# Optimization experiments

Measured on AMD Instinct MI355X. Metric: run time of the kernel, lower is better.

The kernel has to match this reference:

```python
import jax, jax.numpy as jnp
import numpy as np

HID = 128      # hidden_dim (= head_dim since num_heads = 1)
NR = 64        # num_radial
CUT = 10.0     # cutoff
K = 32         # k_neighbors
E = 8192       # number of edges
N = 2048       # number of nodes
DIN = 2 * HID + NR + 1  # attention MLP input dim
LN_EPS = 1e-5


def setup_inputs() -> dict:
    key = jax.random.key(0)
    ks = jax.random.split(key, 16)
    def lin(k, i, o):
        # xavier-ish scaling
        return (jax.random.normal(k, (i, o), jnp.float32) / np.sqrt(i)).astype(jnp.float32)
    return {
        "edge_features": jax.random.normal(ks[0], (E, HID), jnp.float32),
        "edge_coords": jax.random.normal(ks[1], (E, 3), jnp.float32),
        "node_coords": jax.random.normal(ks[2], (N, 3), jnp.float32) * 3.0,
        "Wq": lin(ks[4], HID, HID), "Wk": lin(ks[5], HID, HID), "Wv": lin(ks[6], HID, HID),
        "W1": lin(ks[7], DIN, HID), "b1": jnp.zeros((HID,), jnp.float32),
        "W2": lin(ks[8], HID, HID), "b2": jnp.zeros((HID,), jnp.float32),
        "W3": lin(ks[9], HID, 1), "b3": jnp.zeros((1,), jnp.float32),
        "Wg1": lin(ks[10], HID, HID), "bg1": jnp.zeros((HID,), jnp.float32),
        "Wg2": lin(ks[11], HID, 1), "bg2": jnp.zeros((1,), jnp.float32),
        "Wo": lin(ks[12], HID, HID), "bo": jnp.zeros((HID,), jnp.float32),
        "gamma": jnp.ones((HID,), jnp.float32), "beta": jnp.zeros((HID,), jnp.float32),
        "centers": jnp.linspace(0.0, CUT, NR, dtype=jnp.float32),
        "widths": jnp.full((NR,), 0.5, jnp.float32),
        "edge_index": jax.random.randint(ks[3], (2, E), 0, N, jnp.int32),
    }


def _forward(ef, ec, nc, Wq, Wk, Wv, W1, b1, W2, b2, W3, b3,
             Wg1, bg1, Wg2, bg2, Wo, bo, gamma, beta, centers, widths, edge_index):
    silu = jax.nn.silu
    # edge center coordinates: [E,3]
    cen = (nc[edge_index[0]] + nc[edge_index[1]]) * 0.5
    # pairwise squared distances via gram trick (monotone in distance -> same topk)
    n2 = jnp.sum(cen * cen, axis=-1)
    d2 = n2[:, None] + n2[None, :] - 2.0 * (cen @ cen.T)          # [E,E]
    _, idx = jax.lax.top_k(-d2, K)                                # [E,K] nearest edge centers
    # gathered geometry
    coord_diff = cen[:, None, :] - cen[idx]                       # [E,K,3]
    dist = jnp.sqrt(jnp.sum(coord_diff * coord_diff, axis=-1))    # [E,K]
    in_cut = dist <= CUT                                          # [E,K]
    # RBF (cutoff mask applied as in RadialBasisFunction)
    rbf = jnp.exp(-widths * (dist[..., None] - centers) ** 2) * in_cut[..., None].astype(jnp.float32)  # [E,K,NR]
    # projections (num_heads = 1 -> head_dim = HID)
    q = ef @ Wq                                                   # [E,HID]
    k = ef @ Wk
    v = ef @ Wv
    kj = k[idx]                                                   # [E,K,HID]
    dot = jnp.einsum('ed,ekd->ek', q, kj)                         # [E,K]
    # attention MLP on [q_i, k_j, rbf, dot]
    qb = jnp.broadcast_to(q[:, None, :], (E, K, HID))
    mlp_in = jnp.concatenate([qb, kj, rbf, dot[..., None]], axis=-1)  # [E,K,DIN]
    h = silu(mlp_in @ W1 + b1)
    h = silu(h @ W2 + b2)
    raw = (h @ W3 + b3)[..., 0]                                   # [E,K]
    # scores: MLP output inside cutoff, else left at 0 (as in the torch loop)
    scores = jnp.where(in_cut, raw, 0.0)
    # softmax over the FULL row of length E: the (E-K) non-neighbor entries are 0
    m = jnp.maximum(jnp.max(scores, axis=1), 0.0)                 # [E]
    ex = jnp.exp(scores - m[:, None])                             # [E,K]
    Z = jnp.sum(ex, axis=1) + (E - K) * jnp.exp(-m)               # [E]
    w = ex / Z[:, None]                                           # [E,K] weights at neighbors only
    # feature update: only neighbor entries are accumulated
    weighted_v = jnp.einsum('ek,ekd->ed', w, v[idx])              # [E,HID]
    updated = ef + weighted_v
    # coordinate gates from v
    gates = jax.nn.sigmoid(silu(v @ Wg1 + bg1) @ Wg2 + bg2)       # [E,1]
    gj = gates[idx][..., 0]                                       # [E,K]
    coord_update = jnp.einsum('ek,ekc->ec', w * gj, coord_diff)   # [E,3]
    updated_coords = ec + coord_update
    # output projection + residual + LayerNorm
    x = ef + (updated @ Wo + bo)
    mu = jnp.mean(x, axis=-1, keepdims=True)
    var = jnp.mean((x - mu) ** 2, axis=-1, keepdims=True)
    feat_out = (x - mu) * jax.lax.rsqrt(var + LN_EPS) * gamma + beta
    return feat_out, updated_coords


def reference(edge_features, edge_coords, node_coords, Wq, Wk, Wv, W1, b1, W2, b2, W3, b3,
              Wg1, bg1, Wg2, bg2, Wo, bo, gamma, beta, centers, widths, edge_index):
    return _forward(edge_features, edge_coords, node_coords, Wq, Wk, Wv, W1, b1, W2, b2,
                    W3, b3, Wg1, bg1, Wg2, bg2, Wo, bo, gamma, beta, centers, widths, edge_index)
```

## Files before the change

kernel.cpp:

```cpp
#include <hip/hip_runtime.h>
#include <math.h>

#define E_N   8192
#define HID   128
#define NRAD  64
#define KNB   32
#define CUTF  10.0f
#define LNEPS 1e-5f

typedef unsigned short u16;
typedef unsigned int   u32;
typedef unsigned long long u64;
typedef __bf16 bf16x8 __attribute__((ext_vector_type(8)));
typedef u16    u16x8  __attribute__((ext_vector_type(8)));
typedef float  f32x4  __attribute__((ext_vector_type(4)));

__device__ __forceinline__ u16 f2bf(float f) {
  __bf16 h = (__bf16)f;
  return __builtin_bit_cast(u16, h);
}
__device__ __forceinline__ float bf2f(u16 v) {
  return __uint_as_float(((u32)v) << 16);
}

__device__ __forceinline__ u64 shflx64(u64 v, int m) {
  int lo = __shfl_xor((int)(v & 0xffffffffull), m, 64);
  int hi = __shfl_xor((int)(v >> 32), m, 64);
  return ((u64)(unsigned)hi << 32) | (unsigned)lo;
}

__device__ __forceinline__ u32 d2key(const float4 me, const float4 c) {
  float dot = fmaf(me.x, c.x, fmaf(me.y, c.y, me.z * c.z));
  float d2  = fmaf(-2.0f, dot, me.w + c.w);
  u32 u = __float_as_uint(d2);
  return u ^ (((u32)((int)u >> 31)) | 0x80000000u);
}

__global__ __launch_bounds__(256) void k_pre(
    const float* __restrict__ W1, const float* __restrict__ W2,
    const float* __restrict__ Wq, const float* __restrict__ Wk,
    const float* __restrict__ Wv, const float* __restrict__ Wg1,
    const float* __restrict__ nc, const int* __restrict__ ei,
    u16* __restrict__ Wt1r, u16* __restrict__ Wt2,
    u16* __restrict__ Wqt, u16* __restrict__ Wkt, u16* __restrict__ Wvt,
    u16* __restrict__ Wqct, u16* __restrict__ Wkct, u16* __restrict__ Wvgt,
    float4* __restrict__ cen4) {
  const int b = blockIdx.x, t = threadIdx.x;
  if (b < 128) {
    if (t < 64)       Wt1r[b*64 + t]      = f2bf(W1[(256+t)*HID + b]);
    else if (t < 192) Wt2[b*HID + (t-64)] = f2bf(W2[(t-64)*HID + b]);
  } else if (b < 256) {
    const int r = b - 128, o = t & 127;
    float a = 0.f;
    if (t < 128) {
      #pragma unroll 8
      for (int m = 0; m < 128; ++m) a = fmaf(Wq[r*128+m], W1[m*128+o], a);
      Wqct[o*128 + r] = f2bf(a);
    } else {
      #pragma unroll 8
      for (int m = 0; m < 128; ++m) a = fmaf(Wk[r*128+m], W1[(128+m)*128+o], a);
      Wkct[o*128 + r] = f2bf(a);
    }
  } else if (b < 384) {
    const int r = b - 256;
    if (t < 128) {
      float a = 0.f;
      #pragma unroll 8
      for (int m = 0; m < 128; ++m) a = fmaf(Wv[r*128+m], Wg1[m*128+t], a);
      Wvgt[t*128 + r] = f2bf(a);
    }
  } else if (b < 512) {
    const int c = b - 384;
    if (t < 128) Wqt[c*128 + t]       = f2bf(Wq[t*128 + c]);
    else         Wkt[c*128 + (t-128)] = f2bf(Wk[(t-128)*128 + c]);
  } else if (b < 640) {
    const int c = b - 512;
    if (t < 128) Wvt[c*128 + t] = f2bf(Wv[t*128 + c]);
  } else {
    const int e = (b - 640)*256 + t;
    if (e < E_N) {
      int a = ei[e], bb = ei[E_N + e];
      float x = (nc[a*3+0] + nc[bb*3+0]) * 0.5f;
      float y = (nc[a*3+1] + nc[bb*3+1]) * 0.5f;
      float z = (nc[a*3+2] + nc[bb*3+2]) * 0.5f;
      cen4[e] = make_float4(x, y, z, x*x + y*y + z*z);
    }
  }
}

__global__ __launch_bounds__(256) void k_topk(const float4* __restrict__ cen4,
                                              int* __restrict__ idxo) {
  const int row0 = blockIdx.x * 8;
  const int t = threadIdx.x;
  const int lane = t & 63, w = t >> 6;
  __shared__ __align__(16) u32 smin[8][256];
  __shared__ __align__(16) u64 comp[2048];
  __shared__ u32 sU[8];
  __shared__ u32 scnt, scnt_r[8];
  __shared__ u64 wred[4];
  __shared__ u64 winner;

  if (t == 0) scnt = 0;
  if (t < 8) scnt_r[t] = 0;

  float4 me[8];
  #pragma unroll
  for (int r = 0; r < 8; ++r) me[r] = cen4[row0 + r];

  u32 mn[8];
  #pragma unroll
  for (int r = 0; r < 8; ++r) mn[r] = 0xFFFFFFFFu;
  for (int s = 0; s < 32; ++s) {
    float4 c = cen4[t + (s << 8)];
    #pragma unroll
    for (int r = 0; r < 8; ++r) {
      u32 k = d2key(me[r], c);
      mn[r] = k < mn[r] ? k : mn[r];
    }
  }
  #pragma unroll
  for (int r = 0; r < 8; ++r) smin[r][t] = mn[r];
  __syncthreads();

  #pragma unroll
  for (int rr = 0; rr < 2; ++rr) {
    const int r = w*2 + rr;
    uint4 vv = *(const uint4*)&smin[r][lane*4];
    u32 P = 0;
    u32 rem = 31;
    #pragma unroll 1
    for (int b = 31; b >= 12; --b) {
      u32 bit = 1u << b;
      bool pm0 = ((u64)(vv.x ^ P) >> (b+1)) == 0ull;
      bool pm1 = ((u64)(vv.y ^ P) >> (b+1)) == 0ull;
      bool pm2 = ((u64)(vv.z ^ P) >> (b+1)) == 0ull;
      bool pm3 = ((u64)(vv.w ^ P) >> (b+1)) == 0ull;
      u32 c0 = (u32)__popcll(__ballot(pm0 && !(vv.x & bit)))
             + (u32)__popcll(__ballot(pm1 && !(vv.y & bit)))
             + (u32)__popcll(__ballot(pm2 && !(vv.z & bit)))
             + (u32)__popcll(__ballot(pm3 && !(vv.w & bit)));
      if (rem >= c0) { P |= bit; rem -= c0; }
    }
    if (lane == 0) sU[r] = P | 0xFFFu;
  }
  __syncthreads();

  u32 Ur[8];
  #pragma unroll
  for (int r = 0; r < 8; ++r) Ur[r] = sU[r];
  for (int s = 0; s < 32; ++s) {
    float4 c = cen4[t + (s << 8)];
    #pragma unroll
    for (int r = 0; r < 8; ++r) {
      u32 k = d2key(me[r], c);
      if (k <= Ur[r]) {
        u32 pos = atomicAdd(&scnt, 1u);
        atomicAdd(&scnt_r[r], 1u);
        if (pos < 2048u)
          comp[pos] = ((u64)r << 45) | (((u64)k) << 13) | (u32)(t + (s << 8));
      }
    }
  }
  __syncthreads();
  const int cnt = (int)scnt;

  if (cnt <= 2048) {
    u32 off[8];
    off[0] = 0;
    #pragma unroll
    for (int r = 1; r < 8; ++r) off[r] = off[r-1] + scnt_r[r-1];
    for (int i = t; i < cnt; i += 256) {
      u64 mev = comp[i];
      int rk = 0;
      int j2 = 0;
      for (; j2 + 2 <= cnt; j2 += 2) {
        ulonglong2 pr = *(const ulonglong2*)&comp[j2];
        rk += (pr.x < mev) ? 1 : 0;
        rk += (pr.y < mev) ? 1 : 0;
      }
      if (j2 < cnt) rk += (comp[j2] < mev) ? 1 : 0;
      int r = (int)(mev >> 45);
      int rank = rk - (int)off[r];
      if (rank < KNB) idxo[(row0 + r)*KNB + rank] = (int)(mev & 0x1FFFull);
    }
  } else {
    for (int r = 0; r < 8; ++r) {
      float4 mer = cen4[row0 + r];
      u32 taken = 0;
      for (int kk2 = 0; kk2 < KNB; ++kk2) {
        u64 lk = 0xFFFFFFFFFFFFFFFFull;
        for (int s = 0; s < 32; ++s) {
          if (taken & (1u << s)) continue;
          float4 c = cen4[t + (s << 8)];
          u64 kx = (((u64)d2key(mer, c)) << 13) | (u32)(t + (s << 8));
          lk = kx < lk ? kx : lk;
        }
        #pragma unroll
        for (int m = 1; m < 64; m <<= 1) {
          u64 o = shflx64(lk, m);
          lk = o < lk ? o : lk;
        }
        if (lane == 0) wred[w] = lk;
        __syncthreads();
        if (t == 0) {
          u64 w0 = wred[0] < wred[1] ? wred[0] : wred[1];
          u64 w1 = wred[2] < wred[3] ? wred[2] : wred[3];
          winner = w0 < w1 ? w0 : w1;
          idxo[(row0 + r)*KNB + kk2] = (int)(winner & 0x1FFFull);
        }
        __syncthreads();
        u64 jw = winner & 0x1FFFull;
        if (((u32)jw & 255u) == (u32)t) taken |= 1u << ((u32)jw >> 8);
        __syncthreads();
      }
    }
  }
}

__global__ __launch_bounds__(256) void k_qkv(const float* __restrict__ ef,
    const u16* __restrict__ Wqt, const u16* __restrict__ Wkt, const u16* __restrict__ Wvt,
    const u16* __restrict__ Wqct, const u16* __restrict__ Wkct, const u16* __restrict__ Wvgt,
    const float* __restrict__ b1, const float* __restrict__ bg1,
    const float* __restrict__ Wg2, const float* __restrict__ bg2,
    float* __restrict__ qf, float* __restrict__ qW1,
    u16* __restrict__ kjp, u16* __restrict__ vfb, float* __restrict__ gates) {
  __shared__ u16 sE[32*128];
  __shared__ float spart[4][32];
  const int t = threadIdx.x;
  const int w = t >> 6, l = t & 63;
  const int l15 = l & 15, l4 = l >> 4;
  const int e0 = blockIdx.x * 32;
  const int colw = w * 32;

  {
    const int srow = t >> 3, sb = t & 7;
    const float4* src = (const float4*)(ef + (size_t)(e0 + srow)*HID + sb*16);
    #pragma unroll
    for (int g = 0; g < 2; ++g) {
      float4 v0 = src[g*2], v1 = src[g*2+1];
      u16x8 vv;
      vv[0]=f2bf(v0.x); vv[1]=f2bf(v0.y); vv[2]=f2bf(v0.z); vv[3]=f2bf(v0.w);
      vv[4]=f2bf(v1.x); vv[5]=f2bf(v1.y); vv[6]=f2bf(v1.z); vv[7]=f2bf(v1.w);
      int widx = (srow*128 + sb*16 + g*8) ^ ((srow & 7) << 3);
      *(u16x8*)(&sE[widx]) = vv;
    }
  }
  __syncthreads();

  bf16x8 afq[2][4];
  #pragma unroll
  for (int rt = 0; rt < 2; ++rt) {
    int row = rt*16 + l15;
    #pragma unroll
    for (int ks = 0; ks < 4; ++ks) {
      int aidx = (row*128 + ks*32 + l4*8) ^ ((row & 7) << 3);
      afq[rt][ks] = *(const bf16x8*)(&sE[aidx]);
    }
  }

  f32x4 a2[2][2];
  auto gemm_panel = [&](const u16* __restrict__ P) {
    #pragma unroll
    for (int rt = 0; rt < 2; ++rt)
      #pragma unroll
      for (int ct = 0; ct < 2; ++ct) a2[rt][ct] = (f32x4){0.f,0.f,0.f,0.f};
    #pragma unroll
    for (int ks = 0; ks < 4; ++ks) {
      bf16x8 bfr[2];
      #pragma unroll
      for (int ct = 0; ct < 2; ++ct)
        bfr[ct] = *(const bf16x8*)(&P[(colw + ct*16 + l15)*128 + ks*32 + l4*8]);
      #pragma unroll
      for (int rt = 0; rt < 2; ++rt)
        #pragma unroll
        for (int ct = 0; ct < 2; ++ct)
          a2[rt][ct] = __builtin_amdgcn_mfma_f32_16x16x32_bf16(afq[rt][ks], bfr[ct], a2[rt][ct], 0, 0, 0);
    }
  };

  gemm_panel(Wqt);
  #pragma unroll
  for (int rt = 0; rt < 2; ++rt)
    #pragma unroll
    for (int r = 0; r < 4; ++r) {
      size_t e = e0 + rt*16 + l4*4 + r;
      #pragma unroll
      for (int ct = 0; ct < 2; ++ct)
        qf[e*HID + colw + ct*16 + l15] = a2[rt][ct][r];
    }
  gemm_panel(Wkt);
  #pragma unroll
  for (int rt = 0; rt < 2; ++rt)
    #pragma unroll
    for (int r = 0; r < 4; ++r) {
      size_t e = e0 + rt*16 + l4*4 + r;
      #pragma unroll
      for (int ct = 0; ct < 2; ++ct)
        kjp[e*256 + 128 + colw + ct*16 + l15] = f2bf(a2[rt][ct][r]);
    }
  gemm_panel(Wvt);
  #pragma unroll
  for (int rt = 0; rt < 2; ++rt)
    #pragma unroll
    for (int r = 0; r < 4; ++r) {
      size_t e = e0 + rt*16 + l4*4 + r;
      #pragma unroll
      for (int ct = 0; ct < 2; ++ct)
        vfb[e*HID + colw + ct*16 + l15] = f2bf(a2[rt][ct][r]);
    }
  gemm_panel(Wqct);
  {
    float b1r[2];
    #pragma unroll
    for (int ct = 0; ct < 2; ++ct) b1r[ct] = b1[colw + ct*16 + l15];
    #pragma unroll
    for (int rt = 0; rt < 2; ++rt)
      #pragma unroll
      for (int r = 0; r < 4; ++r) {
        size_t e = e0 + rt*16 + l4*4 + r;
        #pragma unroll
        for (int ct = 0; ct < 2; ++ct)
          qW1[e*HID + colw + ct*16 + l15] = a2[rt][ct][r] + b1r[ct];
      }
  }
  gemm_panel(Wkct);
  #pragma unroll
  for (int rt = 0; rt < 2; ++rt)
    #pragma unroll
    for (int r = 0; r < 4; ++r) {
      size_t e = e0 + rt*16 + l4*4 + r;
      #pragma unroll
      for (int ct = 0; ct < 2; ++ct)
        kjp[e*256 + colw + ct*16 + l15] = f2bf(a2[rt][ct][r]);
    }
  gemm_panel(Wvgt);
  {
    float bgr[2], w3r[2];
    #pragma unroll
    for (int ct = 0; ct < 2; ++ct) {
      int col = colw + ct*16 + l15;
      bgr[ct] = bg1[col]; w3r[ct] = Wg2[col];
    }
    #pragma unroll
    for (int rt = 0; rt < 2; ++rt)
      #pragma unroll
      for (int r = 0; r < 4; ++r) {
        float part = 0.f;
        #pragma unroll
        for (int ct = 0; ct < 2; ++ct) {
          float x = a2[rt][ct][r] + bgr[ct];
          float g = x / (1.0f + __expf(-x));
          part = fmaf(g, w3r[ct], part);
        }
        part += __shfl_xor(part, 1, 64);
        part += __shfl_xor(part, 2, 64);
        part += __shfl_xor(part, 4, 64);
        part += __shfl_xor(part, 8, 64);
        if (l15 == 0) spart[w][rt*16 + l4*4 + r] = part;
      }
  }
  __syncthreads();
  if (t < 32)
    gates[e0 + t] = 1.0f / (1.0f + __expf(-(spart[0][t] + spart[1][t] + spart[2][t] + spart[3][t] + bg2[0])));
}

__global__ __launch_bounds__(512) void k_mega(
    const int* __restrict__ idx,
    const float* __restrict__ qf,
    const float4* __restrict__ cen4,
    const float* __restrict__ qW1, const u16* __restrict__ kjp,
    const u16* __restrict__ vfb, const float* __restrict__ gates,
    const u16* __restrict__ Wt1r, const u16* __restrict__ Wt2,
    const float* __restrict__ W1,
    const float* __restrict__ b2, const float* __restrict__ W3,
    const float* __restrict__ b3,
    const float* __restrict__ centers, const float* __restrict__ widths,
    const float* __restrict__ ef, const float* __restrict__ ec,
    const float* __restrict__ Wo, const float* __restrict__ bo,
    const float* __restrict__ gamma, const float* __restrict__ beta,
    float* __restrict__ outf, float* __restrict__ outc) {
  __shared__ u16 sH[128*128];
  __shared__ u16 sA[128*64];
  float* spart = (float*)sA;
  float* sUpd  = (float*)sA + 512;
  float* swk   = (float*)sA + 1024;
  float* sred  = (float*)sA + 1152;
  __shared__ float sQW[4][128];
  __shared__ float sDot[128];
  __shared__ float sDist[128];
  __shared__ int   sIdx[128];

  const int t  = threadIdx.x;
  const int w  = t >> 6, l = t & 63;
  const int l15 = l & 15, l4 = l >> 4;
  const int c4 = w & 3, rh = w >> 2;
  const int rowbase = blockIdx.x * 128;
  const int eBase = rowbase >> 5;

  const int srow = t >> 2, sb = t & 3;
  const int sp = rowbase + srow;
  const int se = sp >> 5;
  const int sj = idx[sp];
  {
    const u16x8* kw = (const u16x8*)(kjp + (size_t)sj*256 + sb*32);
    #pragma unroll
    for (int g = 0; g < 4; ++g) {
      int widx = (srow*128 + sb*32 + g*8) ^ ((srow & 7) << 3);
      *(u16x8*)(&sH[widx]) = kw[g];
    }
  }
  const u16x8* kb = (const u16x8*)(kjp + (size_t)sj*256 + 128 + sb*32);
  const float4* q4 = (const float4*)(qf + (size_t)se*HID) + sb*8;
  float dt = 0.f;
  #pragma unroll
  for (int i = 0; i < 4; ++i) {
    u16x8 kv8 = kb[i];
    float4 qa = q4[i*2], qb = q4[i*2+1];
    dt += bf2f(kv8[0])*qa.x + bf2f(kv8[1])*qa.y + bf2f(kv8[2])*qa.z + bf2f(kv8[3])*qa.w
        + bf2f(kv8[4])*qb.x + bf2f(kv8[5])*qb.y + bf2f(kv8[6])*qb.z + bf2f(kv8[7])*qb.w;
  }
  dt += __shfl_xor(dt, 1, 64);
  dt += __shfl_xor(dt, 2, 64);
  float4 ce = cen4[se], cj = cen4[sj];
  float ddx = ce.x - cj.x, ddy = ce.y - cj.y, ddz = ce.z - cj.z;
  const float sdist = sqrtf(ddx*ddx + ddy*ddy + ddz*ddz);
  const float sincut = (sdist <= CUTF) ? 1.0f : 0.0f;
  if (sb == 0) { sDot[srow] = dt; sDist[srow] = sdist; }
  {
    u16 tmp[16];
    #pragma unroll
    for (int i4 = 0; i4 < 4; ++i4) {
      float4 cc = *(const float4*)(centers + sb*16 + i4*4);
      float4 ww = *(const float4*)(widths  + sb*16 + i4*4);
      float c4v[4] = {cc.x,cc.y,cc.z,cc.w}, w4[4] = {ww.x,ww.y,ww.z,ww.w};
      #pragma unroll
      for (int jj = 0; jj < 4; ++jj) {
        float df = sdist - c4v[jj];
        tmp[i4*4+jj] = f2bf(__expf(-w4[jj]*df*df) * sincut);
      }
    }
    #pragma unroll
    for (int g = 0; g < 2; ++g) {
      u16x8 vv;
      #pragma unroll
      for (int jj = 0; jj < 8; ++jj) vv[jj] = tmp[g*8+jj];
      int widx = (srow*64 + sb*16 + g*8) ^ ((srow & 7) << 3);
      *(u16x8*)(&sA[widx]) = vv;
    }
  }
  sQW[t >> 7][t & 127] = qW1[(size_t)(eBase + (t >> 7))*HID + (t & 127)];
  if (t < 128) sIdx[t] = idx[rowbase + t];

  u32 vp[16];
  {
    const int eh2 = t >> 7, colp = t & 127;
    const int ib = rowbase + eh2*32;
    #pragma unroll
    for (int kk = 0; kk < 16; ++kk) {
      int j0 = idx[ib + 2*kk], j1 = idx[ib + 2*kk + 1];
      u32 a = vfb[(size_t)j0*HID + colp];
      u32 b = vfb[(size_t)j1*HID + colp];
      vp[kk] = a | (b << 16);
    }
  }
  __syncthreads();

  f32x4 acc[4][2];
  #pragma unroll
  for (int rt = 0; rt < 4; ++rt)
    #pragma unroll
    for (int ct = 0; ct < 2; ++ct) acc[rt][ct] = (f32x4){0.f,0.f,0.f,0.f};

  #pragma unroll
  for (int ks = 0; ks < 2; ++ks) {
    bf16x8 af[4], bfr[2];
    #pragma unroll
    for (int rt = 0; rt < 4; ++rt) {
      int row = rh*64 + rt*16 + l15;
      int aidx = (row*64 + ks*32 + l4*8) ^ ((row & 7) << 3);
      af[rt] = *(const bf16x8*)(&sA[aidx]);
    }
    #pragma unroll
    for (int ct = 0; ct < 2; ++ct) {
      int col = c4*32 + ct*16 + l15;
      bfr[ct] = *(const bf16x8*)(&Wt1r[col*64 + ks*32 + l4*8]);
    }
    #pragma unroll
    for (int rt = 0; rt < 4; ++rt)
      #pragma unroll
      for (int ct = 0; ct < 2; ++ct)
        acc[rt][ct] = __builtin_amdgcn_mfma_f32_16x16x32_bf16(af[rt], bfr[ct], acc[rt][ct], 0, 0, 0);
  }

  {
    float w320[2];
    #pragma unroll
    for (int ct = 0; ct < 2; ++ct) {
      int col = c4*32 + ct*16 + l15;
      w320[ct] = W1[320*HID + col];
    }
    #pragma unroll
    for (int rt = 0; rt < 4; ++rt) {
      #pragma unroll
      for (int r = 0; r < 4; ++r) {
        int row = rh*64 + rt*16 + l4*4 + r;
        float dv = sDot[row];
        int eh = row >> 5;
        #pragma unroll
        for (int ct = 0; ct < 2; ++ct) {
          int col = c4*32 + ct*16 + l15;
          int hidx = (row*128 + col) ^ ((row & 7) << 3);
          float x = acc[rt][ct][r] + sQW[eh][col] + bf2f(sH[hidx]) + dv*w320[ct];
          float h = x / (1.0f + __expf(-x));
          sH[hidx] = f2bf(h);
        }
      }
    }
  }
  __syncthreads();

  #pragma unroll
  for (int rt = 0; rt < 4; ++rt)
    #pragma unroll
    for (int ct = 0; ct < 2; ++ct) acc[rt][ct] = (f32x4){0.f,0.f,0.f,0.f};

  #pragma unroll
  for (int ks = 0; ks < 4; ++ks) {
    bf16x8 af[4], bfr[2];
    #pragma unroll
    for (int rt = 0; rt < 4; ++rt) {
      int row = rh*64 + rt*16 + l15;
      int aidx = (row*128 + ks*32 + l4*8) ^ ((row & 7) << 3);
      af[rt] = *(const bf16x8*)(&sH[aidx]);
    }
    #pragma unroll
    for (int ct = 0; ct < 2; ++ct) {
      int col = c4*32 + ct*16 + l15;
      bfr[ct] = *(const bf16x8*)(&Wt2[col*128 + ks*32 + l4*8]);
    }
    #pragma unroll
    for (int rt = 0; rt < 4; ++rt)
      #pragma unroll
      for (int ct = 0; ct < 2; ++ct)
        acc[rt][ct] = __builtin_amdgcn_mfma_f32_16x16x32_bf16(af[rt], bfr[ct], acc[rt][ct], 0, 0, 0);
  }

  {
    float b2r[2], w3r[2];
    #pragma unroll
    for (int ct = 0; ct < 2; ++ct) {
      int col = c4*32 + ct*16 + l15;
      b2r[ct] = b2[col]; w3r[ct] = W3[col];
    }
    #pragma unroll
    for (int rt = 0; rt < 4; ++rt) {
      #pragma unroll
      for (int r = 0; r < 4; ++r) {
        float part = 0.f;
        #pragma unroll
        for (int ct = 0; ct < 2; ++ct) {
          float x = acc[rt][ct][r] + b2r[ct];
          float h = x / (1.0f + __expf(-x));
          part = fmaf(h, w3r[ct], part);
        }
        part += __shfl_xor(part, 1, 64);
        part += __shfl_xor(part, 2, 64);
        part += __shfl_xor(part, 4, 64);
        part += __shfl_xor(part, 8, 64);
        if (l15 == 0) spart[c4*128 + rh*64 + rt*16 + l4*4 + r] = part;
      }
    }
  }
  __syncthreads();

  if (w < 4 && l < 32) {
    const int eh = w;
    const int row = eh*32 + l;
    float raw = spart[row] + spart[128 + row] + spart[256 + row] + spart[384 + row] + b3[0];
    float sc = (sDist[row] <= CUTF) ? raw : 0.0f;
    float m = sc;
    #pragma unroll
    for (int mm = 1; mm < 32; mm <<= 1) m = fmaxf(m, __shfl_xor(m, mm, 64));
    m = fmaxf(m, 0.0f);
    float ex = __expf(sc - m);
    float Z = ex;
    #pragma unroll
    for (int mm = 1; mm < 32; mm <<= 1) Z += __shfl_xor(Z, mm, 64);
    Z += 8160.0f * __expf(-m);
    float wv = ex / Z;
    swk[eh*32 + l] = wv;
    int j = sIdx[row];
    float g = wv * gates[j];
    float4 cee = cen4[eBase + eh], cjj = cen4[j];
    float cx = g*(cee.x - cjj.x), cy = g*(cee.y - cjj.y), cz = g*(cee.z - cjj.z);
    #pragma unroll
    for (int mm = 1; mm < 32; mm <<= 1) {
      cx += __shfl_xor(cx, mm, 64);
      cy += __shfl_xor(cy, mm, 64);
      cz += __shfl_xor(cz, mm, 64);
    }
    if (l == 0) {
      int e = eBase + eh;
      outc[e*3+0] = ec[e*3+0] + cx;
      outc[e*3+1] = ec[e*3+1] + cy;
      outc[e*3+2] = ec[e*3+2] + cz;
    }
  }
  __syncthreads();

  {
    const int eh = t >> 7, col = t & 127;
    float acc2 = 0.f;
    #pragma unroll
    for (int kk = 0; kk < 16; ++kk) {
      acc2 = fmaf(swk[eh*32 + 2*kk],     bf2f((u16)(vp[kk] & 0xffffu)), acc2);
      acc2 = fmaf(swk[eh*32 + 2*kk + 1], bf2f((u16)(vp[kk] >> 16)),     acc2);
    }
    sUpd[eh*128 + col] = ef[(size_t)(eBase + eh)*HID + col] + acc2;
  }
  __syncthreads();

  {
    const int eh = t >> 7, o = t & 127;
    const int e = eBase + eh;
    float accw = 0.f;
    #pragma unroll 8
    for (int d = 0; d < 128; ++d)
      accw = fmaf(sUpd[eh*128 + d], Wo[d*128 + o], accw);
    float x = ef[(size_t)e*HID + o] + accw + bo[o];
    float s1 = x, s2 = x*x;
    #pragma unroll
    for (int m = 1; m < 64; m <<= 1) {
      s1 += __shfl_xor(s1, m, 64);
      s2 += __shfl_xor(s2, m, 64);
    }
    if (l == 0) { sred[w*2+0] = s1; sred[w*2+1] = s2; }
    __syncthreads();
    float t1 = sred[(eh*2)*2+0] + sred[(eh*2+1)*2+0];
    float t2 = sred[(eh*2)*2+1] + sred[(eh*2+1)*2+1];
    float mu = t1 * (1.0f/128.0f);
    float var = t2 * (1.0f/128.0f) - mu*mu;
    float rs = rsqrtf(var + LNEPS);
    outf[(size_t)e*HID + o] = (x - mu)*rs*gamma[o] + beta[o];
  }
}

extern "C" void kernel_launch(void* const* d_in, const int* in_sizes, int n_in,
                              void* d_out, int out_size, void* d_ws, size_t ws_size,
                              hipStream_t stream) {
  const float* ef   = (const float*)d_in[0];
  const float* ec   = (const float*)d_in[1];
  const float* nc   = (const float*)d_in[2];
  const float* Wq   = (const float*)d_in[3];
  const float* Wk   = (const float*)d_in[4];
  const float* Wv   = (const float*)d_in[5];
  const float* W1   = (const float*)d_in[6];
  const float* b1   = (const float*)d_in[7];
  const float* W2   = (const float*)d_in[8];
  const float* b2   = (const float*)d_in[9];
  const float* W3   = (const float*)d_in[10];
  const float* b3   = (const float*)d_in[11];
  const float* Wg1  = (const float*)d_in[12];
  const float* bg1  = (const float*)d_in[13];
  const float* Wg2  = (const float*)d_in[14];
  const float* bg2  = (const float*)d_in[15];
  const float* Wo   = (const float*)d_in[16];
  const float* bo   = (const float*)d_in[17];
  const float* gamma= (const float*)d_in[18];
  const float* beta = (const float*)d_in[19];
  const float* centers = (const float*)d_in[20];
  const float* widths  = (const float*)d_in[21];
  const int*   eidx    = (const int*)d_in[22];

  float* outf = (float*)d_out;
  float* outc = outf + (size_t)E_N * HID;

  float4* cen4 = (float4*)d_ws;
  u16*   kjp   = (u16*)(cen4 + E_N);
  u16*   vfb   = kjp + (size_t)E_N*256;
  u16*   Wt1r  = vfb + (size_t)E_N*128;
  u16*   Wt2   = Wt1r + 128*64;
  u16*   Wqt   = Wt2  + 128*128;
  u16*   Wkt   = Wqt  + 128*128;
  u16*   Wvt   = Wkt  + 128*128;
  u16*   Wqct  = Wvt  + 128*128;
  u16*   Wkct  = Wqct + 128*128;
  u16*   Wvgt  = Wkct + 128*128;
  int*   idx   = (int*)(Wvgt + 128*128);
  float* qf    = (float*)(idx + E_N*KNB);
  float* qW1   = qf + (size_t)E_N*HID;
  float* gates = qW1 + (size_t)E_N*HID;

  k_pre<<<672, 256, 0, stream>>>(W1, W2, Wq, Wk, Wv, Wg1, nc, eidx,
                                 Wt1r, Wt2, Wqt, Wkt, Wvt, Wqct, Wkct, Wvgt, cen4);
  k_topk<<<E_N/8, 256, 0, stream>>>(cen4, idx);
  k_qkv<<<E_N/32, 256, 0, stream>>>(ef, Wqt, Wkt, Wvt, Wqct, Wkct, Wvgt,
                                    b1, bg1, Wg2, bg2, qf, qW1, kjp, vfb, gates);
  k_mega<<<E_N*KNB/128, 512, 0, stream>>>(idx, qf, cen4, qW1, kjp, vfb, gates, Wt1r, Wt2,
                                          W1, b2, W3, b3, centers, widths, ef, ec,
                                          Wo, bo, gamma, beta, outf, outc);
}
```

Baseline: 198.9 us.

## Spatially bin edges and remap mega-kernel blocks for neighbor gather locality

Adds a single-block counting sort that buckets edge centers into a coarse 3D grid and writes a permutation of edge ids. The mega kernel then processes edges in that spatial order and also swizzles block ids across groups of eight, so blocks running at the same time touch nearby edges whose neighbor rows (kjp, vfb, gates) overlap in cache. This is meant to cut global/L2 traffic from the random neighbor gathers. It costs an extra serial launch on one block and an indirection through eperm on every per-edge load and store.

```diff
diff --git a/kernel.cpp b/kernel.cpp
--- a/kernel.cpp
+++ b/kernel.cpp
@@ -85,6 +85,46 @@
       float z = (nc[a*3+2] + nc[bb*3+2]) * 0.5f;
       cen4[e] = make_float4(x, y, z, x*x + y*y + z*z);
     }
+  }
+}
+
+__global__ __launch_bounds__(256) void k_sort(const float4* __restrict__ cen4,
+                                              int* __restrict__ eperm) {
+  __shared__ u32 hist[256], base[256], wred[4];
+  const int t = threadIdx.x;
+  const int lane = t & 63, w = t >> 6;
+  hist[t] = 0;
+  __syncthreads();
+  u32 keys[32];
+  #pragma unroll
+  for (int s = 0; s < 32; ++s) {
+    float4 c = cen4[t + (s << 8)];
+    int qx = (int)((c.x + 8.0f) * 0.5f);  qx = qx < 0 ? 0 : (qx > 7 ? 7 : qx);
+    int qy = (int)((c.y + 8.0f) * 0.5f);  qy = qy < 0 ? 0 : (qy > 7 ? 7 : qy);
+    int qz = (int)((c.z + 8.0f) * 0.25f); qz = qz < 0 ? 0 : (qz > 3 ? 3 : qz);
+    u32 key = ((u32)qx << 5) | ((u32)qy << 2) | (u32)qz;
+    keys[s] = key;
+    atomicAdd(&hist[key], 1u);
+  }
+  __syncthreads();
+  u32 h = hist[t];
+  int inc = (int)h;
+  #pragma unroll
+  for (int off = 1; off < 64; off <<= 1) {
+    int v = __shfl_up(inc, off, 64);
+    if (lane >= off) inc += v;
+  }
+  if (lane == 63) wred[w] = (u32)inc;
+  __syncthreads();
+  u32 woff = 0;
+  #pragma unroll
+  for (int ww = 0; ww < 4; ++ww) woff += (ww < w) ? wred[ww] : 0u;
+  base[t] = woff + (u32)inc - h;
+  __syncthreads();
+  #pragma unroll
+  for (int s = 0; s < 32; ++s) {
+    u32 pos = atomicAdd(&base[keys[s]], 1u);
+    eperm[pos] = t + (s << 8);
   }
 }
 
@@ -365,7 +405,7 @@
 }
 
 __global__ __launch_bounds__(512) void k_mega(
-    const int* __restrict__ idx,
+    const int* __restrict__ idx, const int* __restrict__ eperm,
     const float* __restrict__ qf,
     const float4* __restrict__ cen4,
     const float* __restrict__ qW1, const u16* __restrict__ kjp,
@@ -389,28 +429,29 @@
   __shared__ float sDot[128];
   __shared__ float sDist[128];
   __shared__ int   sIdx[128];
+  __shared__ int   sEid[4];
 
   const int t  = threadIdx.x;
   const int w  = t >> 6, l = t & 63;
   const int l15 = l & 15, l4 = l >> 4;
   const int c4 = w & 3, rh = w >> 2;
-  const int rowbase = blockIdx.x * 128;
-  const int eBase = rowbase >> 5;
+  const int g  = (blockIdx.x & 7) * 256 + (blockIdx.x >> 3);
+  const int gb = g * 4;
 
   const int srow = t >> 2, sb = t & 3;
-  const int sp = rowbase + srow;
-  const int se = sp >> 5;
-  const int sj = idx[sp];
+  const int myE = eperm[gb + (srow >> 5)];
+  const int sj  = idx[myE*KNB + (srow & 31)];
+  if (t < 4) sEid[t] = eperm[gb + t];
   {
     const u16x8* kw = (const u16x8*)(kjp + (size_t)sj*256 + sb*32);
     #pragma unroll
-    for (int g = 0; g < 4; ++g) {
-      int widx = (srow*128 + sb*32 + g*8) ^ ((srow & 7) << 3);
-      *(u16x8*)(&sH[widx]) = kw[g];
+    for (int gg = 0; gg < 4; ++gg) {
+      int widx = (srow*128 + sb*32 + gg*8) ^ ((srow & 7) << 3);
+      *(u16x8*)(&sH[widx]) = kw[gg];
     }
   }
   const u16x8* kb = (const u16x8*)(kjp + (size_t)sj*256 + 128 + sb*32);
-  const float4* q4 = (const float4*)(qf + (size_t)se*HID) + sb*8;
+  const float4* q4 = (const float4*)(qf + (size_t)myE*HID) + sb*8;
   float dt = 0.f;
   #pragma unroll
   for (int i = 0; i < 4; ++i) {
@@ -421,7 +462,7 @@
   }
   dt += __shfl_xor(dt, 1, 64);
   dt += __shfl_xor(dt, 2, 64);
-  float4 ce = cen4[se], cj = cen4[sj];
+  float4 ce = cen4[myE], cj = cen4[sj];
   float ddx = ce.x - cj.x, ddy = ce.y - cj.y, ddz = ce.z - cj.z;
   const float sdist = sqrtf(ddx*ddx + ddy*ddy + ddz*ddz);
   const float sincut = (sdist <= CUTF) ? 1.0f : 0.0f;
@@ -440,24 +481,27 @@
       }
     }
     #pragma unroll
-    for (int g = 0; g < 2; ++g) {
+    for (int gg = 0; gg < 2; ++gg) {
       u16x8 vv;
       #pragma unroll
-      for (int jj = 0; jj < 8; ++jj) vv[jj] = tmp[g*8+jj];
-      int widx = (srow*64 + sb*16 + g*8) ^ ((srow & 7) << 3);
+      for (int jj = 0; jj < 8; ++jj) vv[jj] = tmp[gg*8+jj];
+      int widx = (srow*64 + sb*16 + gg*8) ^ ((srow & 7) << 3);
       *(u16x8*)(&sA[widx]) = vv;
     }
   }
-  sQW[t >> 7][t & 127] = qW1[(size_t)(eBase + (t >> 7))*HID + (t & 127)];
-  if (t < 128) sIdx[t] = idx[rowbase + t];
+  {
+    const int qe = eperm[gb + (t >> 7)];
+    sQW[t >> 7][t & 127] = qW1[(size_t)qe*HID + (t & 127)];
+  }
+  if (t < 128) sIdx[t] = idx[eperm[gb + (t >> 5)]*KNB + (t & 31)];
 
   u32 vp[16];
   {
-    const int eh2 = t >> 7, colp = t & 127;
-    const int ib = rowbase + eh2*32;
+    const int pe = eperm[gb + (t >> 7)];
+    const int colp = t & 127;
     #pragma unroll
     for (int kk = 0; kk < 16; ++kk) {
-      int j0 = idx[ib + 2*kk], j1 = idx[ib + 2*kk + 1];
+      int j0 = idx[pe*KNB + 2*kk], j1 = idx[pe*KNB + 2*kk + 1];
       u32 a = vfb[(size_t)j0*HID + colp];
       u32 b = vfb[(size_t)j1*HID + colp];
       vp[kk] = a | (b << 16);
@@ -589,10 +633,11 @@
     Z += 8160.0f * __expf(-m);
     float wv = ex / Z;
     swk[eh*32 + l] = wv;
+    int e = sEid[eh];
     int j = sIdx[row];
-    float g = wv * gates[j];
-    float4 cee = cen4[eBase + eh], cjj = cen4[j];
-    float cx = g*(cee.x - cjj.x), cy = g*(cee.y - cjj.y), cz = g*(cee.z - cjj.z);
+    float g2 = wv * gates[j];
+    float4 cee = cen4[e], cjj = cen4[j];
+    float cx = g2*(cee.x - cjj.x), cy = g2*(cee.y - cjj.y), cz = g2*(cee.z - cjj.z);
     #pragma unroll
     for (int mm = 1; mm < 32; mm <<= 1) {
       cx += __shfl_xor(cx, mm, 64);
@@ -600,7 +645,6 @@
       cz += __shfl_xor(cz, mm, 64);
     }
     if (l == 0) {
-      int e = eBase + eh;
       outc[e*3+0] = ec[e*3+0] + cx;
       outc[e*3+1] = ec[e*3+1] + cy;
       outc[e*3+2] = ec[e*3+2] + cz;
@@ -616,13 +660,13 @@
       acc2 = fmaf(swk[eh*32 + 2*kk],     bf2f((u16)(vp[kk] & 0xffffu)), acc2);
       acc2 = fmaf(swk[eh*32 + 2*kk + 1], bf2f((u16)(vp[kk] >> 16)),     acc2);
     }
-    sUpd[eh*128 + col] = ef[(size_t)(eBase + eh)*HID + col] + acc2;
+    sUpd[eh*128 + col] = ef[(size_t)sEid[eh]*HID + col] + acc2;
   }
   __syncthreads();
 
   {
     const int eh = t >> 7, o = t & 127;
-    const int e = eBase + eh;
+    const int e = sEid[eh];
     float accw = 0.f;
     #pragma unroll 8
     for (int d = 0; d < 128; ++d)
@@ -687,16 +731,18 @@
   u16*   Wkct  = Wqct + 128*128;
   u16*   Wvgt  = Wkct + 128*128;
   int*   idx   = (int*)(Wvgt + 128*128);
-  float* qf    = (float*)(idx + E_N*KNB);
+  int*   eperm = idx + E_N*KNB;
+  float* qf    = (float*)(eperm + E_N);
   float* qW1   = qf + (size_t)E_N*HID;
   float* gates = qW1 + (size_t)E_N*HID;
 
   k_pre<<<672, 256, 0, stream>>>(W1, W2, Wq, Wk, Wv, Wg1, nc, eidx,
                                  Wt1r, Wt2, Wqt, Wkt, Wvt, Wqct, Wkct, Wvgt, cen4);
+  k_sort<<<1, 256, 0, stream>>>(cen4, eperm);
   k_topk<<<E_N/8, 256, 0, stream>>>(cen4, idx);
   k_qkv<<<E_N/32, 256, 0, stream>>>(ef, Wqt, Wkt, Wvt, Wqct, Wkct, Wvgt,
                                     b1, bg1, Wg2, bg2, qf, qW1, kjp, vfb, gates);
-  k_mega<<<E_N*KNB/128, 512, 0, stream>>>(idx, qf, cen4, qW1, kjp, vfb, gates, Wt1r, Wt2,
-                                          W1, b2, W3, b3, centers, widths, ef, ec,
-                                          Wo, bo, gamma, beta, outf, outc);
-}
+  k_mega<<<E_N*KNB/128, 512, 0, stream>>>(idx, eperm, qf, cen4, qW1, kjp, vfb, gates,
+                                          Wt1r, Wt2, W1, b2, W3, b3, centers, widths,
+                                          ef, ec, Wo, bo, gamma, beta, outf, outc);
+}
```

Measured after the change: 210.1 us. +5.6%, slower.
